# Optimization experiments

Measured on AMD Instinct MI355X. Metric: run time of the kernel, lower is better.

## Reference

```python
import jax, jax.numpy as jnp
import numpy as np

B = 2; R_PER = 512; R = B * R_PER; RM_PER = 128; RM = B * RM_PER
NUM_CLASSES = 81; C = 256
IMG_H = 800.0; IMG_W = 800.0
SCALES = (0.25, 0.125, 0.0625, 0.03125)  # FPN strides 4,8,16,32
REG_W = (10.0, 10.0, 5.0, 5.0)
LOG_1000_16 = 4.135166556742356  # math.log(1000/16)


def _prep(c, size):
    # torchvision roi_align (aligned=False) coordinate handling
    valid = (c > -1.0) & (c < size)
    c = jnp.clip(c, 0.0, size - 1.0)
    lo = jnp.clip(jnp.floor(c), 0.0, size - 2.0).astype(jnp.int32)
    frac = c - lo.astype(c.dtype)
    return lo, frac, valid


def roi_align(feat, boxes, b_idx, scale, out_size, sr=2):
    # feat [B,C,H,W], boxes [R,4] in image coords, b_idx [R] int
    _, Cn, H, W = feat.shape
    bb = boxes * scale
    x1, y1 = bb[:, 0], bb[:, 1]
    rw = jnp.maximum(bb[:, 2] - x1, 1.0)
    rh = jnp.maximum(bb[:, 3] - y1, 1.0)
    n = out_size * sr
    g = (jnp.arange(n, dtype=feat.dtype) + 0.5) / (sr * out_size)
    ys = y1[:, None] + rh[:, None] * g[None, :]  # [R,n]
    xs = x1[:, None] + rw[:, None] * g[None, :]
    y0, ly, yv = _prep(ys, H)
    x0, lx, xv = _prep(xs, W)
    bi = b_idx[:, None, None]
    yy = y0[:, :, None]; xx = x0[:, None, :]
    f00 = feat[bi, :, yy, xx]          # [R,n,n,C]
    f01 = feat[bi, :, yy, xx + 1]
    f10 = feat[bi, :, yy + 1, xx]
    f11 = feat[bi, :, yy + 1, xx + 1]
    ly_ = ly[:, :, None, None]; lx_ = lx[:, None, :, None]
    v = (f00 * (1 - ly_) * (1 - lx_) + f01 * (1 - ly_) * lx_
         + f10 * ly_ * (1 - lx_) + f11 * ly_ * lx_)
    mask = (yv[:, :, None] & xv[:, None, :]).astype(v.dtype)[..., None]
    v = v * mask
    Rn = boxes.shape[0]
    v = v.reshape(Rn, out_size, sr, out_size, sr, Cn).mean(axis=(2, 4))
    return jnp.transpose(v, (0, 3, 1, 2))  # [R,C,out,out]


def multiscale_roi_align(feats, boxes, b_idx, out_size):
    area = jnp.maximum(boxes[:, 2] - boxes[:, 0], 0.0) * jnp.maximum(boxes[:, 3] - boxes[:, 1], 0.0)
    lvl = jnp.clip(jnp.floor(4.0 + jnp.log2(jnp.sqrt(area) / 224.0 + 1e-6)), 2.0, 5.0).astype(jnp.int32) - 2
    out = 0.0
    for i, (f, s) in enumerate(zip(feats, SCALES)):
        out = out + roi_align(f, boxes, b_idx, s, out_size) * (lvl == i)[:, None, None, None].astype(f.dtype)
    return out


def decode_boxes(deltas, boxes):
    # deltas [R,K,4], boxes [R,4]
    wx, wy, ww, wh = REG_W
    w = boxes[:, 2] - boxes[:, 0]; h = boxes[:, 3] - boxes[:, 1]
    cx = boxes[:, 0] + 0.5 * w; cy = boxes[:, 1] + 0.5 * h
    dx = deltas[..., 0] / wx; dy = deltas[..., 1] / wy
    dw = jnp.minimum(deltas[..., 2] / ww, LOG_1000_16)
    dh = jnp.minimum(deltas[..., 3] / wh, LOG_1000_16)
    pcx = dx * w[:, None] + cx[:, None]; pcy = dy * h[:, None] + cy[:, None]
    pw = jnp.exp(dw) * w[:, None]; ph = jnp.exp(dh) * h[:, None]
    out = jnp.stack([pcx - 0.5 * pw, pcy - 0.5 * ph, pcx + 0.5 * pw, pcy + 0.5 * ph], axis=-1)
    hi = jnp.array([IMG_W, IMG_H, IMG_W, IMG_H], dtype=out.dtype)
    return jnp.clip(out, 0.0, hi)  # process_box clip-to-image


def conv3x3(x, w, b):
    y = jax.lax.conv_general_dilated(x, w, (1, 1), ((1, 1), (1, 1)),
                                     dimension_numbers=('NCHW', 'OIHW', 'NCHW'))
    return jax.nn.relu(y + b[None, :, None, None])


def _forward(feat0, feat1, feat2, feat3, proposals, fc1_w, fc1_b, fc2_w, fc2_b,
             cls_w, cls_b, bbox_w, bbox_b, mconv_w, mconv_b, deconv_w, deconv_b,
             mlogit_w, mlogit_b, batch_idx):
    feats = (feat0, feat1, feat2, feat3)
    # box branch
    bf = multiscale_roi_align(feats, proposals, batch_idx, 7).reshape(R, -1)  # [R, 256*49]
    x = jax.nn.relu(bf @ fc1_w.T + fc1_b)
    x = jax.nn.relu(x @ fc2_w.T + fc2_b)
    scores = jax.nn.softmax(x @ cls_w.T + cls_b, axis=-1)          # [R,81]
    deltas = (x @ bbox_w.T + bbox_b).reshape(R, NUM_CLASSES, 4)
    boxes = decode_boxes(deltas, proposals)                        # [R,81,4]
    # mask branch on top-of-list detections (RM_PER per image), box at argmax fg class
    idx_m = jnp.concatenate([jnp.arange(RM_PER), R_PER + jnp.arange(RM_PER)])
    labels = jnp.argmax(scores[idx_m, 1:], axis=-1) + 1            # [RM]
    mboxes = boxes[idx_m, labels]                                  # [RM,4]
    mf = multiscale_roi_align(feats, mboxes, batch_idx[idx_m], 14)  # [RM,256,14,14]
    for i in range(4):
        mf = conv3x3(mf, mconv_w[i], mconv_b[i])
    # ConvTranspose2d k=2 s=2 (non-overlapping) as einsum, PyTorch IOHW weights
    t = jnp.einsum('bcij,copq->boipjq', mf, deconv_w).reshape(RM, C, 28, 28)
    t = jax.nn.relu(t + deconv_b[None, :, None, None])
    ml = jnp.einsum('bchw,oc->bohw', t, mlogit_w) + mlogit_b[None, :, None, None]
    masks = jax.nn.sigmoid(ml[jnp.arange(RM), labels])             # [RM,28,28]
    return scores, boxes, masks


def setup_inputs() -> dict:
    key = jax.random.key(0)
    ks = jax.random.split(key, 16)
    rn = lambda i, shape, s=1.0: jax.random.normal(ks[i], shape, dtype=jnp.float32) * s
    feat0 = rn(0, (B, C, 200, 200))
    feat1 = rn(1, (B, C, 100, 100))
    feat2 = rn(2, (B, C, 50, 50))
    feat3 = rn(3, (B, C, 25, 25))
    u = jax.random.uniform(ks[4], (R, 4), dtype=jnp.float32)
    x1 = u[:, 0] * (IMG_W - 64.0); y1 = u[:, 1] * (IMG_H - 64.0)
    w = 16.0 + u[:, 2] * 300.0; h = 16.0 + u[:, 3] * 300.0
    proposals = jnp.stack([x1, y1, jnp.minimum(x1 + w, IMG_W), jnp.minimum(y1 + h, IMG_H)], axis=1)
    batch_idx = jnp.repeat(jnp.arange(B, dtype=jnp.int32), R_PER)
    return dict(
        feat0=feat0, feat1=feat1, feat2=feat2, feat3=feat3,
        proposals=proposals,
        fc1_w=rn(5, (1024, C * 49), 0.01), fc1_b=jnp.zeros(1024, jnp.float32),
        fc2_w=rn(6, (1024, 1024), 0.02), fc2_b=jnp.zeros(1024, jnp.float32),
        cls_w=rn(7, (NUM_CLASSES, 1024), 0.02), cls_b=jnp.zeros(NUM_CLASSES, jnp.float32),
        bbox_w=rn(8, (NUM_CLASSES * 4, 1024), 0.01), bbox_b=jnp.zeros(NUM_CLASSES * 4, jnp.float32),
        mconv_w=rn(9, (4, C, C, 3, 3), 0.03), mconv_b=jnp.zeros((4, C), jnp.float32),
        deconv_w=rn(10, (C, C, 2, 2), 0.06), deconv_b=jnp.zeros(C, jnp.float32),
        mlogit_w=rn(11, (NUM_CLASSES, C), 0.06), mlogit_b=jnp.zeros(NUM_CLASSES, jnp.float32),
        batch_idx=batch_idx,
    )


def reference(feat0, feat1, feat2, feat3, proposals, fc1_w, fc1_b, fc2_w, fc2_b,
              cls_w, cls_b, bbox_w, bbox_b, mconv_w, mconv_b, deconv_w, deconv_b,
              mlogit_w, mlogit_b, batch_idx):
    return _forward(feat0, feat1, feat2, feat3, proposals, fc1_w, fc1_b, fc2_w, fc2_b,
                    cls_w, cls_b, bbox_w, bbox_b, mconv_w, mconv_b, deconv_w, deconv_b,
                    mlogit_w, mlogit_b, batch_idx)
```

## Files before the change

kernel.cpp:

```cpp
#include <hip/hip_runtime.h>


#define NUM_CLASSES 81
#define CDIM 256
#define RTOT 1024
#define RMASK 256
#define LOG1000_16 4.135166556742356f

typedef _Float16 half8v __attribute__((ext_vector_type(8)));
typedef _Float16 half4v __attribute__((ext_vector_type(4)));
typedef float    float4v __attribute__((ext_vector_type(4)));
typedef float    float2a4 __attribute__((ext_vector_type(2), aligned(4)));

__device__ __forceinline__ void gload_lds16(const void* g, void* l) {
    __builtin_amdgcn_global_load_lds(
        (const __attribute__((address_space(1))) void*)g,
        (__attribute__((address_space(3))) void*)l, 16, 0, 0);
}

__global__ __launch_bounds__(256) void roi_align7_kernel(
    const float* __restrict__ f0, const float* __restrict__ f1,
    const float* __restrict__ f2, const float* __restrict__ f3,
    const float* __restrict__ props, const int* __restrict__ bidx,
    _Float16* __restrict__ bf_h, _Float16* __restrict__ bf_l)
{
    int r  = blockIdx.x;
    int cg = blockIdx.y;
    int t = threadIdx.x;
    if (t >= 196) return;
    int p  = t % 49;
    int cl = t / 49;
    int oy = p / 7, ox = p % 7;

    float x1 = props[r*4+0], y1 = props[r*4+1];
    float x2 = props[r*4+2], y2 = props[r*4+3];
    float area = fmaxf(x2-x1, 0.f) * fmaxf(y2-y1, 0.f);
    float lf = floorf(4.f + log2f(sqrtf(area)/224.f + 1e-6f));
    lf = fminf(fmaxf(lf, 2.f), 5.f);
    int lvl = (int)lf - 2;

    const float* feat; int H, W; float scale;
    if (lvl == 0)      { feat = f0; H = 200; W = 200; scale = 0.25f; }
    else if (lvl == 1) { feat = f1; H = 100; W = 100; scale = 0.125f; }
    else if (lvl == 2) { feat = f2; H = 50;  W = 50;  scale = 0.0625f; }
    else               { feat = f3; H = 25;  W = 25;  scale = 0.03125f; }
    int b = bidx[r];

    float x1s = x1*scale, y1s = y1*scale;
    float rw = fmaxf(x2*scale - x1s, 1.f);
    float rh = fmaxf(y2*scale - y1s, 1.f);

    int   offs[4];
    float w00[4], w01[4], w10[4], w11[4];
    #pragma unroll
    for (int sy = 0; sy < 2; ++sy) {
        int iy = oy*2 + sy;
        float gy = ((float)iy + 0.5f) / 14.f;
        float yc = y1s + rh*gy;
        bool  yv = (yc > -1.f) && (yc < (float)H);
        float ycl = fminf(fmaxf(yc, 0.f), (float)(H-1));
        int   y0  = (int)fminf(floorf(ycl), (float)(H-2));
        float ly  = ycl - (float)y0;
        #pragma unroll
        for (int sx = 0; sx < 2; ++sx) {
            int ix = ox*2 + sx;
            float gx = ((float)ix + 0.5f) / 14.f;
            float xc = x1s + rw*gx;
            bool  xv = (xc > -1.f) && (xc < (float)W);
            float xcl = fminf(fmaxf(xc, 0.f), (float)(W-1));
            int   x0  = (int)fminf(floorf(xcl), (float)(W-2));
            float lx  = xcl - (float)x0;
            float m = (yv && xv) ? 1.f : 0.f;
            int s = sy*2 + sx;
            offs[s] = y0*W + x0;
            w00[s] = (1.f-ly)*(1.f-lx)*m;
            w01[s] = (1.f-ly)*lx*m;
            w10[s] = ly*(1.f-lx)*m;
            w11[s] = ly*lx*m;
        }
    }

    size_t HW = (size_t)H * W;
    #pragma unroll 4
    for (int k = 0; k < 16; ++k) {
        int c = cg*64 + cl + k*4;
        const float* fb = feat + ((size_t)b*CDIM + c) * HW;
        float acc = 0.f;
        #pragma unroll
        for (int s = 0; s < 4; ++s) {
            const float* q = fb + offs[s];
            float2a4 u = *(const float2a4*)q;
            float2a4 v = *(const float2a4*)(q + W);
            acc += w00[s]*u.x + w01[s]*u.y + w10[s]*v.x + w11[s]*v.y;
        }
        float v = acc * 0.25f;
        _Float16 h = (_Float16)v;
        size_t o = (size_t)r*12544 + c*49 + p;
        bf_h[o] = h;
        bf_l[o] = (_Float16)((v - (float)h) * 2048.f);
    }
}

template<int BMODE>
__global__ __launch_bounds__(256, 1) void gemm_fc2(
    const _Float16* __restrict__ Ah, const _Float16* __restrict__ Al,
    const float* __restrict__ B32,
    const _Float16* __restrict__ Bh16, const _Float16* __restrict__ Bl16,
    float* __restrict__ Cp, int K, int KS, int NS)
{
    __shared__ __align__(16) char smem[3*32768];

    int t = threadIdx.x;
    int lane = t & 63, wave = t >> 6;
    int wm = wave >> 1, wn = wave & 1;
    int ln = lane & 15, q = lane >> 4;

    int gx = gridDim.x, gy = gridDim.y;
    int lin = blockIdx.x + gx*(blockIdx.y + gy*blockIdx.z);
    int per = (gx*gy*(int)gridDim.z) >> 3;
    int nl  = (lin & 7)*per + (lin >> 3);
    int bn  = nl % gx;
    int tmp = nl / gx;
    int bm  = tmp % gy;
    int kz  = tmp / gy;

    size_t kbase = (size_t)kz * KS;
    int asub = lane >> 2;
    int achk = (lane & 3) ^ ((lane >> 3) & 3);

    const _Float16* Agh0 = Ah + (size_t)(bm*128 + wave*32 + asub)*K + kbase + achk*8;
    const _Float16* Agh1 = Agh0 + (size_t)16*K;
    const _Float16* Agl0 = Al + (size_t)(bm*128 + wave*32 + asub)*K + kbase + achk*8;
    const _Float16* Agl1 = Agl0 + (size_t)16*K;
    int adst0 = (wave*32 + 0)*32;
    int adst1 = (wave*32 + 16)*32;

    const _Float16 *Bgh0=nullptr, *Bgh1=nullptr, *Bgl0=nullptr, *Bgl1=nullptr;
    const float *Bg0=nullptr, *Bg1=nullptr, *Bg2=nullptr, *Bg3=nullptr;
    int fdst0 = 0;
    if constexpr (BMODE == 1) {
        Bgh0 = Bh16 + (size_t)(bn*128 + wave*32 + asub)*K + kbase + achk*8;
        Bgh1 = Bgh0 + (size_t)16*K;
        Bgl0 = Bl16 + (size_t)(bn*128 + wave*32 + asub)*K + kbase + achk*8;
        Bgl1 = Bgl0 + (size_t)16*K;
    } else {
        int br8  = lane >> 3;
        int bchk = (lane & 7) ^ br8;
        const float* base = B32 + (size_t)(bn*128 + wave*32 + br8)*K + kbase + bchk*4;
        Bg0 = base;
        Bg1 = base + (size_t)8*K;
        Bg2 = base + (size_t)16*K;
        Bg3 = base + (size_t)24*K;
        fdst0 = (wave*32)*32;
    }

    auto AhB = [&](int b){ return (_Float16*)(smem + b*32768); };
    auto AlB = [&](int b){ return (_Float16*)(smem + b*32768 + 8192); };
    auto BhB = [&](int b){ return (_Float16*)(smem + b*32768 + 16384); };
    auto BlB = [&](int b){ return (_Float16*)(smem + b*32768 + 24576); };
    auto BfB = [&](int b){ return (float*)   (smem + b*32768 + 16384); };

    auto dma = [&](int k0, int b) {
        gload_lds16(Agh0 + k0, AhB(b) + adst0);
        gload_lds16(Agh1 + k0, AhB(b) + adst1);
        gload_lds16(Agl0 + k0, AlB(b) + adst0);
        gload_lds16(Agl1 + k0, AlB(b) + adst1);
        if constexpr (BMODE == 1) {
            gload_lds16(Bgh0 + k0, BhB(b) + adst0);
            gload_lds16(Bgh1 + k0, BhB(b) + adst1);
            gload_lds16(Bgl0 + k0, BlB(b) + adst0);
            gload_lds16(Bgl1 + k0, BlB(b) + adst1);
        } else {
            gload_lds16(Bg0 + k0, BfB(b) + fdst0);
            gload_lds16(Bg1 + k0, BfB(b) + fdst0 + 8*32);
            gload_lds16(Bg2 + k0, BfB(b) + fdst0 + 16*32);
            gload_lds16(Bg3 + k0, BfB(b) + fdst0 + 24*32);
        }
    };

    float4v acc1[4][4], acc2[4][4];
    #pragma unroll
    for (int i = 0; i < 4; ++i)
        #pragma unroll
        for (int j = 0; j < 4; ++j) {
            acc1[i][j] = (float4v){0.f,0.f,0.f,0.f};
            acc2[i][j] = (float4v){0.f,0.f,0.f,0.f};
        }

    int cq = (q ^ ((ln >> 1) & 3)) * 8;

    auto compute = [&](int b) {
        const _Float16* ah = AhB(b);
        const _Float16* al = AlB(b);
        half8v afh[4], afl[4], bfh[4], bfl[4];
        #pragma unroll
        for (int i = 0; i < 4; ++i) {
            int ra = (wm*64 + i*16 + ln)*32 + cq;
            afh[i] = *(const half8v*)&ah[ra];
            afl[i] = *(const half8v*)&al[ra];
        }
        if constexpr (BMODE == 1) {
            const _Float16* bh = BhB(b);
            const _Float16* bl = BlB(b);
            #pragma unroll
            for (int j = 0; j < 4; ++j) {
                int rb = (wn*64 + j*16 + ln)*32 + cq;
                bfh[j] = *(const half8v*)&bh[rb];
                bfl[j] = *(const half8v*)&bl[rb];
            }
        } else {
            const float* bfp = BfB(b);
            #pragma unroll
            for (int j = 0; j < 4; ++j) {
                int row = wn*64 + j*16 + ln;
                int c0 = (q*2)   ^ (row & 7);
                int c1 = (q*2+1) ^ (row & 7);
                float4v f0 = *(const float4v*)&bfp[row*32 + c0*4];
                float4v f1 = *(const float4v*)&bfp[row*32 + c1*4];
                #pragma unroll
                for (int e = 0; e < 4; ++e) {
                    _Float16 h0 = (_Float16)f0[e];
                    bfh[j][e] = h0;
                    bfl[j][e] = (_Float16)((f0[e] - (float)h0) * 2048.f);
                    _Float16 h1 = (_Float16)f1[e];
                    bfh[j][4+e] = h1;
                    bfl[j][4+e] = (_Float16)((f1[e] - (float)h1) * 2048.f);
                }
            }
        }
        #pragma unroll
        for (int i = 0; i < 4; ++i) {
            #pragma unroll
            for (int j = 0; j < 4; ++j) {
                acc1[i][j] = __builtin_amdgcn_mfma_f32_16x16x32_f16(
                    afh[i], bfh[j], acc1[i][j], 0, 0, 0);
                acc2[i][j] = __builtin_amdgcn_mfma_f32_16x16x32_f16(
                    afh[i], bfl[j], acc2[i][j], 0, 0, 0);
                acc2[i][j] = __builtin_amdgcn_mfma_f32_16x16x32_f16(
                    afl[i], bfh[j], acc2[i][j], 0, 0, 0);
            }
        }
    };

    int NT = KS / 32;
    dma(0, 0);
    if (NT > 1) dma(32, 1);

    for (int tt = 0; tt < NT; ++tt) {
        if (tt < NT-1) asm volatile("s_waitcnt vmcnt(8)" ::: "memory");
        else           asm volatile("s_waitcnt vmcnt(0)" ::: "memory");
        __builtin_amdgcn_s_barrier();
        asm volatile("" ::: "memory");
        if (tt + 2 < NT) dma((tt+2)*32, (tt+2)%3);
        compute(tt%3);
    }

    float* Cpz = Cp + (size_t)kz*1024*NS;
    #pragma unroll
    for (int i = 0; i < 4; ++i) {
        #pragma unroll
        for (int j = 0; j < 4; ++j) {
            int col = bn*128 + wn*64 + j*16 + ln;
            #pragma unroll
            for (int reg = 0; reg < 4; ++reg) {
                int row = bm*128 + wm*64 + i*16 + q*4 + reg;
                Cpz[(size_t)row*NS + col] =
                    acc1[i][j][reg] + acc2[i][j][reg] * (1.f/2048.f);
            }
        }
    }
}

__global__ __launch_bounds__(256) void fc_reduce_kernel(
    const float* __restrict__ Cp, const float* __restrict__ bias,
    float* __restrict__ out, _Float16* __restrict__ outh,
    _Float16* __restrict__ outl, int nparts, int ns4, int do_relu)
{
    int i = blockIdx.x*256 + threadIdx.x;
    const float4* p = (const float4*)Cp;
    int pstride = 1024*ns4;
    float sx = 0.f, sy = 0.f, sz = 0.f, sw = 0.f;
    for (int j = 0; j < nparts; ++j) {
        float4 s = p[i + j*pstride];
        sx += s.x; sy += s.y; sz += s.z; sw += s.w;
    }
    float4 b4 = ((const float4*)bias)[i & (ns4-1)];
    float4 v;
    v.x = sx + b4.x; v.y = sy + b4.y; v.z = sz + b4.z; v.w = sw + b4.w;
    if (do_relu) {
        v.x = fmaxf(v.x, 0.f); v.y = fmaxf(v.y, 0.f);
        v.z = fmaxf(v.z, 0.f); v.w = fmaxf(v.w, 0.f);
    }
    if (out) ((float4*)out)[i] = v;
    if (outh) {
        float vv[4] = {v.x, v.y, v.z, v.w};
        half4v hh, hl;
        #pragma unroll
        for (int c2 = 0; c2 < 4; ++c2) {
            _Float16 h = (_Float16)vv[c2];
            hh[c2] = h;
            hl[c2] = (_Float16)((vv[c2] - (float)h) * 2048.f);
        }
        ((half4v*)outh)[i] = hh;
        ((half4v*)outl)[i] = hl;
    }
}

__global__ __launch_bounds__(256) void repack_split_kernel(
    const float* __restrict__ w, _Float16* __restrict__ h,
    _Float16* __restrict__ l)
{
    int i = blockIdx.x*256 + threadIdx.x;
    float4 v = ((const float4*)w)[i];
    float vv[4] = {v.x, v.y, v.z, v.w};
    half4v hh, hl;
    #pragma unroll
    for (int c2 = 0; c2 < 4; ++c2) {
        _Float16 hj = (_Float16)vv[c2];
        hh[c2] = hj;
        hl[c2] = (_Float16)((vv[c2] - (float)hj) * 2048.f);
    }
    ((half4v*)h)[i] = hh;
    ((half4v*)l)[i] = hl;
}

__global__ __launch_bounds__(256) void repack_head_kernel(
    const float* __restrict__ cls_w, const float* __restrict__ cls_b,
    const float* __restrict__ bbox_w, const float* __restrict__ bbox_b,
    _Float16* __restrict__ Wcat_h, _Float16* __restrict__ Wcat_l,
    float* __restrict__ bcat)
{
    int i = blockIdx.x*256 + threadIdx.x;
    int row = i >> 10, col = i & 1023;
    float v = 0.f;
    if (row < 81) v = cls_w[row*1024 + col];
    else if (row < 405) v = bbox_w[(row-81)*1024 + col];
    _Float16 h = (_Float16)v;
    Wcat_h[i] = h;
    Wcat_l[i] = (_Float16)((v - (float)h) * 2048.f);
    if (i < 512) {
        float bv = 0.f;
        if (i < 81) bv = cls_b[i];
        else if (i < 405) bv = bbox_b[i-81];
        bcat[i] = bv;
    }
}

__global__ __launch_bounds__(128) void heads_finish_kernel(
    const float* __restrict__ L, const float* __restrict__ props,
    float* __restrict__ scores, float* __restrict__ boxes,
    int* __restrict__ labels, float* __restrict__ mboxes)
{
    __shared__ float lg[NUM_CLASSES];
    __shared__ float red[2];
    __shared__ int slab;
    int r = blockIdx.x, t = threadIdx.x;
    const float* Lr = L + (size_t)r*512;
    if (t < NUM_CLASSES) lg[t] = Lr[t];
    __syncthreads();
    if (t == 0) {
        float mx = lg[0];
        for (int j = 1; j < NUM_CLASSES; ++j) mx = fmaxf(mx, lg[j]);
        red[0] = mx;
    }
    __syncthreads();
    float mx = red[0];
    if (t < NUM_CLASSES) lg[t] = expf(lg[t] - mx);
    __syncthreads();
    if (t == 0) {
        float s = 0.f;
        int best = 1; float bv = lg[1];
        for (int j = 0; j < NUM_CLASSES; ++j) {
            s += lg[j];
            if (j >= 1 && lg[j] > bv) { bv = lg[j]; best = j; }
        }
        red[1] = 1.f/s;
        slab = best;
    }
    __syncthreads();
    if (t < NUM_CLASSES) scores[(size_t)r*NUM_CLASSES + t] = lg[t]*red[1];

    bool sel = (r < 128) || (r >= 512 && r < 640);
    int mi = (r < 128) ? r : r - 384;
    if (t == 0 && sel) labels[mi] = slab;

    if (t < NUM_CLASSES) {
        float px1 = props[r*4+0], py1 = props[r*4+1];
        float px2 = props[r*4+2], py2 = props[r*4+3];
        float pw = px2 - px1, ph = py2 - py1;
        float cx = px1 + 0.5f*pw, cy = py1 + 0.5f*ph;
        const float* dl = Lr + 81 + t*4;
        float d0 = dl[0] * 0.1f;
        float d1 = dl[1] * 0.1f;
        float d2 = fminf(dl[2] * 0.2f, LOG1000_16);
        float d3 = fminf(dl[3] * 0.2f, LOG1000_16);
        float pcx = d0*pw + cx, pcy = d1*ph + cy;
        float qw = expf(d2)*pw, qh = expf(d3)*ph;
        float b0 = fminf(fmaxf(pcx - 0.5f*qw, 0.f), 800.f);
        float b1 = fminf(fmaxf(pcy - 0.5f*qh, 0.f), 800.f);
        float b2 = fminf(fmaxf(pcx + 0.5f*qw, 0.f), 800.f);
        float b3 = fminf(fmaxf(pcy + 0.5f*qh, 0.f), 800.f);
        size_t ob = ((size_t)r*NUM_CLASSES + t)*4;
        boxes[ob+0] = b0; boxes[ob+1] = b1; boxes[ob+2] = b2; boxes[ob+3] = b3;
        if (sel && t == slab) {
            mboxes[mi*4+0] = b0; mboxes[mi*4+1] = b1;
            mboxes[mi*4+2] = b2; mboxes[mi*4+3] = b3;
        }
    }
}

__global__ __launch_bounds__(256) void roi_align14_kernel(
    const float* __restrict__ f0, const float* __restrict__ f1,
    const float* __restrict__ f2, const float* __restrict__ f3,
    const float* __restrict__ mboxes, const int* __restrict__ bidx,
    _Float16* __restrict__ outT)
{
    int mi = blockIdx.x;
    int cg = blockIdx.y;
    int t = threadIdx.x;
    if (t >= 196) return;
    int oy = t / 14, ox = t % 14;

    float x1 = mboxes[mi*4+0], y1 = mboxes[mi*4+1];
    float x2 = mboxes[mi*4+2], y2 = mboxes[mi*4+3];
    float area = fmaxf(x2-x1, 0.f) * fmaxf(y2-y1, 0.f);
    float lf = floorf(4.f + log2f(sqrtf(area)/224.f + 1e-6f));
    lf = fminf(fmaxf(lf, 2.f), 5.f);
    int lvl = (int)lf - 2;

    const float* feat; int H, W; float scale;
    if (lvl == 0)      { feat = f0; H = 200; W = 200; scale = 0.25f; }
    else if (lvl == 1) { feat = f1; H = 100; W = 100; scale = 0.125f; }
    else if (lvl == 2) { feat = f2; H = 50;  W = 50;  scale = 0.0625f; }
    else               { feat = f3; H = 25;  W = 25;  scale = 0.03125f; }
    int ridx = (mi < 128) ? mi : mi + 384;
    int b = bidx[ridx];

    float x1s = x1*scale, y1s = y1*scale;
    float rw = fmaxf(x2*scale - x1s, 1.f);
    float rh = fmaxf(y2*scale - y1s, 1.f);

    int   offs[4];
    float w00[4], w01[4], w10[4], w11[4];
    #pragma unroll
    for (int sy = 0; sy < 2; ++sy) {
        int iy = oy*2 + sy;
        float gy = ((float)iy + 0.5f) / 28.f;
        float yc = y1s + rh*gy;
        bool  yv = (yc > -1.f) && (yc < (float)H);
        float ycl = fminf(fmaxf(yc, 0.f), (float)(H-1));
        int   y0  = (int)fminf(floorf(ycl), (float)(H-2));
        float ly  = ycl - (float)y0;
        #pragma unroll
        for (int sx = 0; sx < 2; ++sx) {
            int ix = ox*2 + sx;
            float gx = ((float)ix + 0.5f) / 28.f;
            float xc = x1s + rw*gx;
            bool  xv = (xc > -1.f) && (xc < (float)W);
            float xcl = fminf(fmaxf(xc, 0.f), (float)(W-1));
            int   x0  = (int)fminf(floorf(xcl), (float)(W-2));
            float lx  = xcl - (float)x0;
            float m = (yv && xv) ? 1.f : 0.f;
            int s = sy*2 + sx;
            offs[s] = y0*W + x0;
            w00[s] = (1.f-ly)*(1.f-lx)*m;
            w01[s] = (1.f-ly)*lx*m;
            w10[s] = ly*(1.f-lx)*m;
            w11[s] = ly*lx*m;
        }
    }

    size_t HW = (size_t)H * W;
    _Float16* orow = outT + ((size_t)mi*196 + t)*CDIM + cg*32;
    const float* fbase = feat + ((size_t)b*CDIM + cg*32) * HW;
    #pragma unroll
    for (int c8 = 0; c8 < 32; c8 += 8) {
        half8v hv;
        #pragma unroll
        for (int cc = 0; cc < 8; ++cc) {
            const float* fb = fbase + (size_t)(c8+cc) * HW;
            float acc = 0.f;
            #pragma unroll
            for (int s = 0; s < 4; ++s) {
                const float* q = fb + offs[s];
                float2a4 u = *(const float2a4*)q;
                float2a4 v = *(const float2a4*)(q + W);
                acc += w00[s]*u.x + w01[s]*u.y + w10[s]*v.x + w11[s]*v.y;
            }
            hv[cc] = (_Float16)(acc * 0.25f);
        }
        *(half8v*)(orow + c8) = hv;
    }
}

__global__ __launch_bounds__(256) void repack_wts_kernel(
    const float* __restrict__ w, _Float16* __restrict__ Wr)
{
    int i = blockIdx.x*256 + threadIdx.x;
    int ci = i & 255;
    int rest = i >> 8;
    int co = rest & 255;
    int rest2 = rest >> 8;
    int tap = rest2 % 9;
    int l = rest2 / 9;
    Wr[i] = (_Float16)w[(((size_t)(l*256 + co)*256 + ci)*9) + tap];
}

__global__ __launch_bounds__(256) void repack_dw_kernel(
    const float* __restrict__ dw, _Float16* __restrict__ Wd)
{
    int i = blockIdx.x*256 + threadIdx.x;
    int n = i >> 8, k = i & 255;
    Wd[i] = (_Float16)dw[(size_t)k*1024 + n];
}

#define PSTR 40

__global__ __launch_bounds__(256, 2) void conv3x3_mfma_kernel(
    const _Float16* __restrict__ inT, const _Float16* __restrict__ Wr,
    const float* __restrict__ bias, _Float16* __restrict__ outT, int layer)
{
    __shared__ _Float16 lin[256*PSTR];

    int t = threadIdx.x;
    int lane = t & 63;
    int wave = t >> 6;
    int ln = lane & 15;
    int q  = lane >> 4;
    int q8 = q*8;
    int r  = blockIdx.x >> 1;
    int bc = blockIdx.x & 1;
    int co_w = bc*128 + wave*32;

    const _Float16* WrL = Wr + (size_t)layer*9*256*256;
    const _Float16* inR = inT + (size_t)r*196*256;

    for (int i = t; i < 256*PSTR; i += 256) lin[i] = (_Float16)0.f;

    float4v acc[13][2];
    #pragma unroll
    for (int nt = 0; nt < 13; ++nt) {
        acc[nt][0] = (float4v){0.f,0.f,0.f,0.f};
        acc[nt][1] = (float4v){0.f,0.f,0.f,0.f};
    }

    for (int ci0 = 0; ci0 < 256; ci0 += 32) {
        __syncthreads();
        for (int idx = t; idx < 784; idx += 256) {
            int p = idx >> 2, g = idx & 3;
            float4 v = *(const float4*)(inR + (size_t)p*256 + ci0 + g*8);
            int row = (p*37450) >> 19;
            int col = p - row*14;
            *(float4*)&lin[((row+1)*16 + (col+1))*PSTR + g*8] = v;
        }
        __syncthreads();

        half8v aw[9][2];
        #pragma unroll
        for (int tap = 0; tap < 9; ++tap) {
            #pragma unroll
            for (int u = 0; u < 2; ++u)
                aw[tap][u] = *(const half8v*)(
                    WrL + ((size_t)tap*256 + co_w + u*16 + ln)*256 + ci0 + q8);
        }

        #pragma unroll
        for (int nt = 0; nt < 13; ++nt) {
            int n = nt*16 + ln;
            int row = (n*37450) >> 19;
            int col = n - row*14;
            int pb = (n < 196) ? (row*16 + col) : 0;
            const _Float16* bp = &lin[pb*PSTR + q8];
            #pragma unroll
            for (int ky = 0; ky < 3; ++ky) {
                #pragma unroll
                for (int kx = 0; kx < 3; ++kx) {
                    half8v bv = *(const half8v*)(bp + (ky*16 + kx)*PSTR);
                    acc[nt][0] = __builtin_amdgcn_mfma_f32_16x16x32_f16(
                        aw[ky*3+kx][0], bv, acc[nt][0], 0, 0, 0);
                    acc[nt][1] = __builtin_amdgcn_mfma_f32_16x16x32_f16(
                        aw[ky*3+kx][1], bv, acc[nt][1], 0, 0, 0);
                }
            }
        }
    }

    #pragma unroll
    for (int u = 0; u < 2; ++u) {
        float4 bi = *(const float4*)&bias[layer*256 + co_w + u*16 + q*4];
        float bia[4] = {bi.x, bi.y, bi.z, bi.w};
        #pragma unroll
        for (int nt = 0; nt < 13; ++nt) {
            int n = nt*16 + ln;
            if (n < 196) {
                half4v hv;
                #pragma unroll
                for (int i = 0; i < 4; ++i)
                    hv[i] = (_Float16)fmaxf(acc[nt][u][i] + bia[i], 0.f);
                *(half4v*)(outT + ((size_t)r*196 + n)*256 + co_w + u*16 + q*4) = hv;
            }
        }
    }
}

#define DSTR 264

template<int NMT>
__device__ __forceinline__ void deconv_pass(
    const _Float16* actL, const _Float16* __restrict__ Wd,
    const float* __restrict__ db, const float* __restrict__ mlw,
    int lab, float (*sred)[4], int wv, int ln, int q, int px0)
{
    float P[NMT][4];
    #pragma unroll
    for (int mt = 0; mt < NMT; ++mt)
        #pragma unroll
        for (int r2 = 0; r2 < 4; ++r2) P[mt][r2] = 0.f;

    for (int c = 0; c < 8; ++c) {
        int n0 = wv*256 + c*32;
        float4v acc[NMT][2];
        #pragma unroll
        for (int mt = 0; mt < NMT; ++mt) {
            acc[mt][0] = (float4v){0.f,0.f,0.f,0.f};
            acc[mt][1] = (float4v){0.f,0.f,0.f,0.f};
        }
        #pragma unroll
        for (int k = 0; k < 8; ++k) {
            const _Float16* wp = Wd + ((size_t)(n0 + ln))*256 + k*32 + q*8;
            half8v b0 = *(const half8v*)wp;
            half8v b1 = *(const half8v*)(wp + 16*256);
            #pragma unroll
            for (int mt = 0; mt < NMT; ++mt) {
                half8v a = *(const half8v*)&actL[(mt*16 + ln)*DSTR + k*32 + q*8];
                acc[mt][0] = __builtin_amdgcn_mfma_f32_16x16x32_f16(
                    a, b0, acc[mt][0], 0, 0, 0);
                acc[mt][1] = __builtin_amdgcn_mfma_f32_16x16x32_f16(
                    a, b1, acc[mt][1], 0, 0, 0);
            }
        }
        #pragma unroll
        for (int j = 0; j < 2; ++j) {
            int n = n0 + j*16 + ln;
            int o = n >> 2;
            float bo = db[o];
            float wl = mlw[lab*256 + o];
            #pragma unroll
            for (int mt = 0; mt < NMT; ++mt)
                #pragma unroll
                for (int r2 = 0; r2 < 4; ++r2)
                    P[mt][r2] += fmaxf(acc[mt][j][r2] + bo, 0.f) * wl;
        }
    }
    #pragma unroll
    for (int mt = 0; mt < NMT; ++mt)
        #pragma unroll
        for (int r2 = 0; r2 < 4; ++r2) {
            float v = P[mt][r2];
            v += __shfl_xor(v, 4);
            v += __shfl_xor(v, 8);
            int px = px0 + mt*16 + q*4 + r2;
            if (ln < 4 && px < 196) atomicAdd(&sred[px][ln], v);
        }
}

__global__ __launch_bounds__(256, 1) void deconv_mask_mfma_kernel(
    const _Float16* __restrict__ mfT, const _Float16* __restrict__ Wd,
    const float* __restrict__ db, const float* __restrict__ mlw,
    const float* __restrict__ mlb, const int* __restrict__ labels,
    float* __restrict__ masks)
{
    __shared__ _Float16 act[112*DSTR];
    __shared__ float sred[196][4];
    int t = threadIdx.x;
    int lane = t & 63, wv = t >> 6, ln = lane & 15, q = lane >> 4;
    int mi = blockIdx.x;
    int lab = labels[mi];

    for (int i = t; i < 784; i += 256) ((float*)sred)[i] = 0.f;

    for (int idx = t; idx < 112*32; idx += 256) {
        int px = idx >> 5, g = idx & 31;
        *(float4*)&act[px*DSTR + g*8] =
            *(const float4*)(mfT + ((size_t)mi*196 + px)*256 + g*8);
    }
    __syncthreads();
    deconv_pass<7>(act, Wd, db, mlw, lab, sred, wv, ln, q, 0);
    __syncthreads();

    for (int idx = t; idx < 84*32; idx += 256) {
        int px = idx >> 5, g = idx & 31;
        *(float4*)&act[px*DSTR + g*8] =
            *(const float4*)(mfT + ((size_t)mi*196 + 112 + px)*256 + g*8);
    }
    __syncthreads();
    deconv_pass<6>(act, Wd, db, mlw, lab, sred, wv, ln, q, 112);
    __syncthreads();

    if (t < 196) {
        float bl = mlb[lab];
        int i2 = t / 14, j2 = t % 14;
        #pragma unroll
        for (int pq = 0; pq < 4; ++pq) {
            float s = sred[t][pq] + bl;
            int h = 2*i2 + (pq >> 1), w2 = 2*j2 + (pq & 1);
            masks[(size_t)mi*784 + h*28 + w2] = 1.f/(1.f + expf(-s));
        }
    }
}

extern "C" void kernel_launch(void* const* d_in, const int* in_sizes, int n_in,
                              void* d_out, int out_size, void* d_ws, size_t ws_size,
                              hipStream_t stream) {
    const float* f0      = (const float*)d_in[0];
    const float* f1      = (const float*)d_in[1];
    const float* f2      = (const float*)d_in[2];
    const float* f3      = (const float*)d_in[3];
    const float* props   = (const float*)d_in[4];
    const float* fc1_w   = (const float*)d_in[5];
    const float* fc1_b   = (const float*)d_in[6];
    const float* fc2_w   = (const float*)d_in[7];
    const float* fc2_b   = (const float*)d_in[8];
    const float* cls_w   = (const float*)d_in[9];
    const float* cls_b   = (const float*)d_in[10];
    const float* bbox_w  = (const float*)d_in[11];
    const float* bbox_b  = (const float*)d_in[12];
    const float* mconv_w = (const float*)d_in[13];
    const float* mconv_b = (const float*)d_in[14];
    const float* dconv_w = (const float*)d_in[15];
    const float* dconv_b = (const float*)d_in[16];
    const float* mlog_w  = (const float*)d_in[17];
    const float* mlog_b  = (const float*)d_in[18];
    const int*   bidx    = (const int*)d_in[19];

    char* wsb = (char*)d_ws;
    _Float16* bf_h = (_Float16*)wsb;
    _Float16* bf_l = (_Float16*)(wsb + 25690112);
    _Float16* fc2h = (_Float16*)wsb;
    _Float16* fc2l = (_Float16*)(wsb + 2097152);
    _Float16* bufA = (_Float16*)wsb;
    _Float16* bufB = (_Float16*)(wsb + 25690112);
    _Float16* x1h  = (_Float16*)(wsb + 51380224);
    _Float16* x1l  = (_Float16*)(wsb + 53477376);
    _Float16* x2h  = (_Float16*)(wsb + 55574528);
    _Float16* x2l  = (_Float16*)(wsb + 57671680);
    int*      labels = (int*)(wsb + 59768832);
    float*    mboxes = (float*)(wsb + 59772928);
    float*    Cp     = (float*)(wsb + 59781120);
    _Float16* Wr     = (_Float16*)(wsb + 59781120);
    _Float16* Wd     = (_Float16*)(wsb + 64499712);
    _Float16* Wcat_h = (_Float16*)(wsb + 76558336);
    _Float16* Wcat_l = (_Float16*)(wsb + 77606912);
    float*    bcat   = (float*)(wsb + 78655488);
    float*    Lh     = (float*)(wsb + 78659584);

    float* scores = (float*)d_out;
    float* boxes  = scores + RTOT*NUM_CLASSES;
    float* masks  = boxes + RTOT*NUM_CLASSES*4;

    roi_align7_kernel<<<dim3(RTOT, 4), 256, 0, stream>>>(
        f0, f1, f2, f3, props, bidx, bf_h, bf_l);

    repack_head_kernel<<<2048, 256, 0, stream>>>(cls_w, cls_b, bbox_w, bbox_b,
                                                 Wcat_h, Wcat_l, bcat);

    gemm_fc2<0><<<dim3(8, 8, 4), 256, 0, stream>>>(
        bf_h, bf_l, fc1_w, nullptr, nullptr, Cp, 12544, 3136, 1024);
    fc_reduce_kernel<<<1024, 256, 0, stream>>>(Cp, fc1_b, nullptr, x1h, x1l,
                                               4, 256, 1);

    repack_split_kernel<<<1024, 256, 0, stream>>>(fc2_w, fc2h, fc2l);

    gemm_fc2<1><<<dim3(8, 8, 4), 256, 0, stream>>>(
        x1h, x1l, nullptr, fc2h, fc2l, Cp, 1024, 256, 1024);
    fc_reduce_kernel<<<1024, 256, 0, stream>>>(Cp, fc2_b, nullptr, x2h, x2l,
                                               4, 256, 1);

    gemm_fc2<1><<<dim3(4, 8, 8), 256, 0, stream>>>(
        x2h, x2l, nullptr, Wcat_h, Wcat_l, Cp, 1024, 128, 512);
    fc_reduce_kernel<<<512, 256, 0, stream>>>(Cp, bcat, Lh, nullptr, nullptr,
                                              8, 128, 0);

    heads_finish_kernel<<<RTOT, 128, 0, stream>>>(Lh, props, scores, boxes,
                                                  labels, mboxes);

    repack_wts_kernel<<<4*9*256, 256, 0, stream>>>(mconv_w, Wr);
    repack_dw_kernel<<<1024, 256, 0, stream>>>(dconv_w, Wd);

    roi_align14_kernel<<<dim3(RMASK, 8), 256, 0, stream>>>(
        f0, f1, f2, f3, mboxes, bidx, bufA);

    conv3x3_mfma_kernel<<<RMASK*2, 256, 0, stream>>>(bufA, Wr, mconv_b, bufB, 0);
    conv3x3_mfma_kernel<<<RMASK*2, 256, 0, stream>>>(bufB, Wr, mconv_b, bufA, 1);
    conv3x3_mfma_kernel<<<RMASK*2, 256, 0, stream>>>(bufA, Wr, mconv_b, bufB, 2);
    conv3x3_mfma_kernel<<<RMASK*2, 256, 0, stream>>>(bufB, Wr, mconv_b, bufA, 3);

    deconv_mask_mfma_kernel<<<RMASK, 256, 0, stream>>>(bufA, Wd, dconv_b, mlog_w,
                                                       mlog_b, labels, masks);
}
```

Baseline: 882.0 us.

## Transpose FPN features to NHWC and gather ROI samples with channel-contiguous loads

Adds a tiled transpose of the four FPN feature maps from NCHW to NHWC in workspace, then new roi_align kernels for the 7x7 and 14x14 poolings. In these, each lane reads float4 channel vectors per bilinear tap, so gathers are contiguous across channels rather than strided across the spatial plane. The change pays for a full transpose of every feature level on each call (about 80MB read and written) and uses more workspace. The new path is chosen only when the workspace is large enough, otherwise the old kernels run.

```diff
diff --git a/kernel.cpp b/kernel.cpp
--- a/kernel.cpp
+++ b/kernel.cpp
@@ -16,6 +16,179 @@
     __builtin_amdgcn_global_load_lds(
         (const __attribute__((address_space(1))) void*)g,
         (__attribute__((address_space(3))) void*)l, 16, 0, 0);
+}
+
+__global__ __launch_bounds__(256) void transpose_nhwc_kernel(
+    const float* __restrict__ in, float* __restrict__ out, int H, int W)
+{
+    __shared__ float tile[64][65];
+    int t = threadIdx.x;
+    int xl = t & 63, cq = t >> 6;
+    int x0 = blockIdx.x * 64;
+    int y  = blockIdx.y;
+    int b  = blockIdx.z >> 2;
+    int c0 = (blockIdx.z & 3) * 64;
+
+    const float* ip = in + (((size_t)(b*CDIM + c0))*H + y)*W + x0;
+    if (x0 + xl < W) {
+        #pragma unroll
+        for (int i = 0; i < 16; ++i) {
+            int cl = cq + i*4;
+            tile[cl][xl] = ip[(size_t)cl*H*W + xl];
+        }
+    }
+    __syncthreads();
+    float* op = out + (((size_t)b*H + y)*W + x0)*CDIM + c0;
+    #pragma unroll
+    for (int i = 0; i < 16; ++i) {
+        int xw = cq + i*4;
+        if (x0 + xw < W)
+            op[(size_t)xw*CDIM + xl] = tile[xl][xw];
+    }
+}
+
+__device__ __forceinline__ void axis_taps(
+    float start, float ext, int o, float invn, int N,
+    float* wgt, int* idx)
+{
+    #pragma unroll
+    for (int s = 0; s < 2; ++s) {
+        int i = o*2 + s;
+        float g = ((float)i + 0.5f) * invn;
+        float c = start + ext*g;
+        float mv = ((c > -1.f) && (c < (float)N)) ? 1.f : 0.f;
+        float cl = fminf(fmaxf(c, 0.f), (float)(N-1));
+        int   i0 = (int)fminf(floorf(cl), (float)(N-2));
+        float l  = cl - (float)i0;
+        wgt[s*2+0] = (1.f-l)*mv;
+        wgt[s*2+1] = l*mv;
+        idx[s*2+0] = i0;
+        idx[s*2+1] = i0+1;
+    }
+}
+
+__global__ __launch_bounds__(256) void roi_align7_nhwc_kernel(
+    const float* __restrict__ fT0, const float* __restrict__ fT1,
+    const float* __restrict__ fT2, const float* __restrict__ fT3,
+    const float* __restrict__ props, const int* __restrict__ bidx,
+    _Float16* __restrict__ bf_h, _Float16* __restrict__ bf_l)
+{
+    __shared__ _Float16 lh[256*49];
+    __shared__ _Float16 ll[256*49];
+    int r = blockIdx.x, t = threadIdx.x;
+    int lane = t & 63, wv = t >> 6;
+
+    float x1 = props[r*4+0], y1 = props[r*4+1];
+    float x2 = props[r*4+2], y2 = props[r*4+3];
+    float area = fmaxf(x2-x1, 0.f) * fmaxf(y2-y1, 0.f);
+    float lf = floorf(4.f + log2f(sqrtf(area)/224.f + 1e-6f));
+    lf = fminf(fmaxf(lf, 2.f), 5.f);
+    int lvl = (int)lf - 2;
+
+    const float* fT; int H, W; float scale;
+    if (lvl == 0)      { fT = fT0; H = 200; W = 200; scale = 0.25f; }
+    else if (lvl == 1) { fT = fT1; H = 100; W = 100; scale = 0.125f; }
+    else if (lvl == 2) { fT = fT2; H = 50;  W = 50;  scale = 0.0625f; }
+    else               { fT = fT3; H = 25;  W = 25;  scale = 0.03125f; }
+    int b = bidx[r];
+    const float* fb = fT + ((size_t)b*H*W)*CDIM + lane*4;
+
+    float x1s = x1*scale, y1s = y1*scale;
+    float rw = fmaxf(x2*scale - x1s, 1.f);
+    float rh = fmaxf(y2*scale - y1s, 1.f);
+
+    for (int p = wv; p < 49; p += 4) {
+        int oy = p / 7, ox = p % 7;
+        float uy[4]; int yr[4];
+        axis_taps(y1s, rh, oy, 1.f/14.f, H, uy, yr);
+        float wx[4]; int xc[4];
+        axis_taps(x1s, rw, ox, 1.f/14.f, W, wx, xc);
+
+        float a0 = 0.f, a1 = 0.f, a2 = 0.f, a3 = 0.f;
+        #pragma unroll
+        for (int a = 0; a < 4; ++a) {
+            const float* rowp = fb + (size_t)(yr[a]*W)*CDIM;
+            #pragma unroll
+            for (int c2 = 0; c2 < 4; ++c2) {
+                float w = uy[a]*wx[c2];
+                float4v v = *(const float4v*)(rowp + xc[c2]*CDIM);
+                a0 += w*v[0]; a1 += w*v[1]; a2 += w*v[2]; a3 += w*v[3];
+            }
+        }
+        float av[4] = {a0, a1, a2, a3};
+        #pragma unroll
+        for (int e = 0; e < 4; ++e) {
+            float vv = av[e]*0.25f;
+            _Float16 h = (_Float16)vv;
+            int c = lane*4 + e;
+            lh[c*49 + p] = h;
+            ll[c*49 + p] = (_Float16)((vv - (float)h)*2048.f);
+        }
+    }
+    __syncthreads();
+    size_t ob = (size_t)r*12544;
+    for (int k = t; k < 12544; k += 256) {
+        bf_h[ob + k] = lh[k];
+        bf_l[ob + k] = ll[k];
+    }
+}
+
+__global__ __launch_bounds__(256) void roi_align14_nhwc_kernel(
+    const float* __restrict__ fT0, const float* __restrict__ fT1,
+    const float* __restrict__ fT2, const float* __restrict__ fT3,
+    const float* __restrict__ mboxes, const int* __restrict__ bidx,
+    _Float16* __restrict__ outT)
+{
+    int mi = blockIdx.x, py = blockIdx.y;
+    int t = threadIdx.x;
+    int lane = t & 63, wv = t >> 6;
+
+    float x1 = mboxes[mi*4+0], y1 = mboxes[mi*4+1];
+    float x2 = mboxes[mi*4+2], y2 = mboxes[mi*4+3];
+    float area = fmaxf(x2-x1, 0.f) * fmaxf(y2-y1, 0.f);
+    float lf = floorf(4.f + log2f(sqrtf(area)/224.f + 1e-6f));
+    lf = fminf(fmaxf(lf, 2.f), 5.f);
+    int lvl = (int)lf - 2;
+
+    const float* fT; int H, W; float scale;
+    if (lvl == 0)      { fT = fT0; H = 200; W = 200; scale = 0.25f; }
+    else if (lvl == 1) { fT = fT1; H = 100; W = 100; scale = 0.125f; }
+    else if (lvl == 2) { fT = fT2; H = 50;  W = 50;  scale = 0.0625f; }
+    else               { fT = fT3; H = 25;  W = 25;  scale = 0.03125f; }
+    int ridx = (mi < 128) ? mi : mi + 384;
+    int b = bidx[ridx];
+    const float* fb = fT + ((size_t)b*H*W)*CDIM + lane*4;
+
+    float x1s = x1*scale, y1s = y1*scale;
+    float rw = fmaxf(x2*scale - x1s, 1.f);
+    float rh = fmaxf(y2*scale - y1s, 1.f);
+
+    for (int pp = wv; pp < 49; pp += 4) {
+        int p = py*49 + pp;
+        int oy = p / 14, ox = p % 14;
+        float uy[4]; int yr[4];
+        axis_taps(y1s, rh, oy, 1.f/28.f, H, uy, yr);
+        float wx[4]; int xc[4];
+        axis_taps(x1s, rw, ox, 1.f/28.f, W, wx, xc);
+
+        float a0 = 0.f, a1 = 0.f, a2 = 0.f, a3 = 0.f;
+        #pragma unroll
+        for (int a = 0; a < 4; ++a) {
+            const float* rowp = fb + (size_t)(yr[a]*W)*CDIM;
+            #pragma unroll
+            for (int c2 = 0; c2 < 4; ++c2) {
+                float w = uy[a]*wx[c2];
+                float4v v = *(const float4v*)(rowp + xc[c2]*CDIM);
+                a0 += w*v[0]; a1 += w*v[1]; a2 += w*v[2]; a3 += w*v[3];
+            }
+        }
+        half4v hv;
+        hv[0] = (_Float16)(a0*0.25f);
+        hv[1] = (_Float16)(a1*0.25f);
+        hv[2] = (_Float16)(a2*0.25f);
+        hv[3] = (_Float16)(a3*0.25f);
+        *(half4v*)(outT + ((size_t)mi*196 + p)*CDIM + lane*4) = hv;
+    }
 }
 
 __global__ __launch_bounds__(256) void roi_align7_kernel(
@@ -753,13 +926,27 @@
     _Float16* Wcat_l = (_Float16*)(wsb + 77606912);
     float*    bcat   = (float*)(wsb + 78655488);
     float*    Lh     = (float*)(wsb + 78659584);
+    float*    fT0    = (float*)(wsb + 80756736);
+    float*    fT1    = (float*)(wsb + 162676736);
+    float*    fT2    = (float*)(wsb + 183156736);
+    float*    fT3    = (float*)(wsb + 188276736);
+    bool nhwc = (ws_size >= 189556736ull);
 
     float* scores = (float*)d_out;
     float* boxes  = scores + RTOT*NUM_CLASSES;
     float* masks  = boxes + RTOT*NUM_CLASSES*4;
 
-    roi_align7_kernel<<<dim3(RTOT, 4), 256, 0, stream>>>(
-        f0, f1, f2, f3, props, bidx, bf_h, bf_l);
+    if (nhwc) {
+        transpose_nhwc_kernel<<<dim3(4, 200, 8), 256, 0, stream>>>(f0, fT0, 200, 200);
+        transpose_nhwc_kernel<<<dim3(2, 100, 8), 256, 0, stream>>>(f1, fT1, 100, 100);
+        transpose_nhwc_kernel<<<dim3(1,  50, 8), 256, 0, stream>>>(f2, fT2,  50,  50);
+        transpose_nhwc_kernel<<<dim3(1,  25, 8), 256, 0, stream>>>(f3, fT3,  25,  25);
+        roi_align7_nhwc_kernel<<<RTOT, 256, 0, stream>>>(
+            fT0, fT1, fT2, fT3, props, bidx, bf_h, bf_l);
+    } else {
+        roi_align7_kernel<<<dim3(RTOT, 4), 256, 0, stream>>>(
+            f0, f1, f2, f3, props, bidx, bf_h, bf_l);
+    }
 
     repack_head_kernel<<<2048, 256, 0, stream>>>(cls_w, cls_b, bbox_w, bbox_b,
                                                  Wcat_h, Wcat_l, bcat);
@@ -787,8 +974,13 @@
     repack_wts_kernel<<<4*9*256, 256, 0, stream>>>(mconv_w, Wr);
     repack_dw_kernel<<<1024, 256, 0, stream>>>(dconv_w, Wd);
 
-    roi_align14_kernel<<<dim3(RMASK, 8), 256, 0, stream>>>(
-        f0, f1, f2, f3, mboxes, bidx, bufA);
+    if (nhwc) {
+        roi_align14_nhwc_kernel<<<dim3(RMASK, 4), 256, 0, stream>>>(
+            fT0, fT1, fT2, fT3, mboxes, bidx, bufA);
+    } else {
+        roi_align14_kernel<<<dim3(RMASK, 8), 256, 0, stream>>>(
+            f0, f1, f2, f3, mboxes, bidx, bufA);
+    }
 
     conv3x3_mfma_kernel<<<RMASK*2, 256, 0, stream>>>(bufA, Wr, mconv_b, bufB, 0);
     conv3x3_mfma_kernel<<<RMASK*2, 256, 0, stream>>>(bufB, Wr, mconv_b, bufA, 1);
```

After: 830.2 us. 1.06x faster.
